# Kernel optimization log

Hardware: AMD Instinct MI355X
Metric: run time of the kernel (lower is better)

## Reference

```python
import jax, jax.numpy as jnp
import numpy as np

DIM = 1024
HEADS = 16
DIM_HEAD = 64
B, N = 2, 2048
EPS_NORM = 1e-12  # F.normalize clamp


def setup_inputs() -> dict:
    key = jax.random.key(0)
    k1, k2, k3 = jax.random.split(key, 3)
    x = jax.random.normal(k1, (B, N, DIM), dtype=jnp.float32)
    gamma = jnp.ones((DIM,), dtype=jnp.float32)
    w_qkv = jax.random.normal(k2, (DIM, 3 * HEADS * DIM_HEAD), dtype=jnp.float32) * (DIM ** -0.5)
    w_out = jax.random.normal(k3, (HEADS * DIM_HEAD, DIM), dtype=jnp.float32) * (DIM ** -0.5)
    return {"x": x, "gamma": gamma, "w_qkv": w_qkv, "w_out": w_out}


def reference(x, gamma, w_qkv, w_out):
    b, n, dim = x.shape
    h, dh = HEADS, DIM_HEAD
    # RMSNorm: F.normalize(x, dim=-1) * sqrt(dim) * gamma
    norm = jnp.maximum(jnp.linalg.norm(x, axis=-1, keepdims=True), EPS_NORM)
    normed = x / norm * (dim ** 0.5) * gamma
    # qkv projection (no bias)
    qkv = normed @ w_qkv  # [b, n, 3*h*dh]
    qkv = qkv.reshape(b, n, 3, h, dh)
    q = qkv[:, :, 0].transpose(0, 2, 1, 3)  # [b, h, n, dh]
    k = qkv[:, :, 1].transpose(0, 2, 1, 3)
    v = qkv[:, :, 2].transpose(0, 2, 1, 3)
    q = q * (dh ** -0.5)
    # attention scores
    sim = jnp.einsum('bhid,bhjd->bhij', q, k)
    mask_value = -jnp.finfo(sim.dtype).max
    # causal mask: triu with offset j - i + 1 (here i == j == n -> offset 1)
    causal_mask = jnp.triu(jnp.ones((n, n), dtype=bool), 1)
    sim = jnp.where(causal_mask, mask_value, sim)
    attn = jax.nn.softmax(sim, axis=-1)
    out = jnp.einsum('bhij,bhjd->bhid', attn, v)
    out = out.transpose(0, 2, 1, 3).reshape(b, n, h * dh)
    return out @ w_out
```

## Files before the change

kernel.cpp:

```cpp
#include <hip/hip_runtime.h>
#include <hip/hip_bf16.h>

typedef unsigned short u16;
using bf16x8 = __attribute__((ext_vector_type(8))) short;
using f32x4  = __attribute__((ext_vector_type(4))) float;
using f32x16 = __attribute__((ext_vector_type(16))) float;
using u32x4  = __attribute__((ext_vector_type(4))) unsigned int;

constexpr int B_ = 2, N_ = 2048, DIM_ = 1024, H_ = 16, DH_ = 64;
constexpr int M_ = B_ * N_;
constexpr int NCQ = 3 * H_ * DH_;

__device__ inline u16 f2bf(float f) {
  union { float f; unsigned u; } v{f};
  unsigned r = v.u + 0x7FFF + ((v.u >> 16) & 1);
  return (u16)(r >> 16);
}

__device__ __forceinline__ void st_pair(u16* p0, u16* p1, float a, float b) {
  unsigned w;
  asm("v_cvt_pk_bf16_f32 %0, %1, %2" : "=v"(w) : "v"(a), "v"(b));
  *p0 = (u16)w;
  *p1 = (u16)(w >> 16);
}

__device__ __forceinline__ void gload16(const u16* g, u16* l) {
  __builtin_amdgcn_global_load_lds(
      (const __attribute__((address_space(1))) unsigned int*)g,
      (__attribute__((address_space(3))) unsigned int*)l, 16, 0, 0);
}

__global__ void __launch_bounds__(256) rmsnorm_kernel(const float* __restrict__ x,
                                                      const float* __restrict__ gamma,
                                                      u16* __restrict__ out) {
  int row = blockIdx.x;
  int t = threadIdx.x;
  const float4 v = reinterpret_cast<const float4*>(x + (size_t)row * DIM_)[t];
  float ss = v.x * v.x + v.y * v.y + v.z * v.z + v.w * v.w;
#pragma unroll
  for (int o = 32; o; o >>= 1) ss += __shfl_down(ss, o, 64);
  __shared__ float partial[4];
  int wid = t >> 6, lane = t & 63;
  if (lane == 0) partial[wid] = ss;
  __syncthreads();
  float tot = partial[0] + partial[1] + partial[2] + partial[3];
  float norm = fmaxf(sqrtf(tot), 1e-12f);
  float scale = 32.0f / norm;
  const float4 g = reinterpret_cast<const float4*>(gamma)[t];
  ushort4 o4;
  o4.x = f2bf(v.x * scale * g.x);
  o4.y = f2bf(v.y * scale * g.y);
  o4.z = f2bf(v.z * scale * g.z);
  o4.w = f2bf(v.w * scale * g.w);
  reinterpret_cast<ushort4*>(out + (size_t)row * DIM_)[t] = o4;
}

__global__ void __launch_bounds__(256) transpose_w_kernel(const float* __restrict__ W,
                                                          u16* __restrict__ WT,
                                                          int K, int Nc) {
  __shared__ float tile[32][33];
  int bc = blockIdx.x * 32;
  int bk = blockIdx.y * 32;
  int tx = threadIdx.x & 31, ty = threadIdx.x >> 5;
#pragma unroll
  for (int r = ty; r < 32; r += 8)
    tile[r][tx] = W[(size_t)(bk + r) * Nc + bc + tx];
  __syncthreads();
#pragma unroll
  for (int r = ty; r < 32; r += 8)
    WT[(size_t)(bc + r) * K + bk + tx] = f2bf(tile[tx][r]);
}

template <int MODE>
__global__ void __launch_bounds__(256) gemm2_kernel(const u16* __restrict__ A,
                                                    const u16* __restrict__ BT,
                                                    void* __restrict__ Cv,
                                                    u16* __restrict__ q_s,
                                                    u16* __restrict__ k_s,
                                                    u16* __restrict__ vt,
                                                    int M, int Nc, int K) {
  __shared__ alignas(16) u16 smem[16384];
  int tid = threadIdx.x;
  int lane = tid & 63, wid = tid >> 6;
  int lr = lane & 15, g = lane >> 4;
  int am0 = (wid >> 1) * 64;
  int bn0 = (wid & 1) * 64;
  int rbase_a = blockIdx.y * 128;
  int rbase_b = blockIdx.x * 128;

  int lineo = tid >> 3;
  int p = tid & 7;
  f32x4 acc[4][4] = {};

#define GSTAGE(base_, src_, rb_, k0_) do {                                           \
    _Pragma("unroll")                                                                \
    for (int c = 0; c < 2; c++) {                                                    \
      int line = c * 32 + lineo;                                                     \
      int sp = p ^ (line & 7);                                                       \
      int row = 2 * line + (sp >> 2);                                                \
      int j = sp & 3;                                                                \
      gload16(src_ + (size_t)(rb_ + row) * K + (k0_) + j * 8,                        \
              (base_) + c * 2048 + wid * 512);                                       \
    }                                                                                \
  } while (0)

#define STAGE(ib_, k0_) do {                                                         \
    GSTAGE(smem + (ib_) * 4096, A, rbase_a, k0_);                                    \
    GSTAGE(smem + 8192 + (ib_) * 4096, BT, rbase_b, k0_);                            \
  } while (0)

  int steps = K >> 5;
  STAGE(0, 0);
  for (int t = 0; t < steps; ++t) {
    int ibuf = t & 1;
    if (t + 1 < steps) {
      STAGE(ibuf ^ 1, (t + 1) * 32);
      asm volatile("s_waitcnt vmcnt(4)" ::: "memory");
    } else {
      asm volatile("s_waitcnt vmcnt(0)" ::: "memory");
    }
    __builtin_amdgcn_s_barrier();
    __builtin_amdgcn_sched_barrier(0);

    const char* ab = (const char*)(smem + ibuf * 4096);
    const char* bb = (const char*)(smem + 8192 + ibuf * 4096);
    bf16x8 a[4], b[4];
#pragma unroll
    for (int mi = 0; mi < 4; mi++) {
      int row = am0 + mi * 16 + lr;
      int byte = (row >> 1) * 128 + ((((row & 1) << 2) + g) ^ ((row >> 1) & 7)) * 16;
      a[mi] = *reinterpret_cast<const bf16x8*>(ab + byte);
    }
#pragma unroll
    for (int ni = 0; ni < 4; ni++) {
      int row = bn0 + ni * 16 + lr;
      int byte = (row >> 1) * 128 + ((((row & 1) << 2) + g) ^ ((row >> 1) & 7)) * 16;
      b[ni] = *reinterpret_cast<const bf16x8*>(bb + byte);
    }
#pragma unroll
    for (int mi = 0; mi < 4; mi++)
#pragma unroll
      for (int ni = 0; ni < 4; ni++)
        acc[mi][ni] = __builtin_amdgcn_mfma_f32_16x16x32_bf16(a[mi], b[ni], acc[mi][ni], 0, 0, 0);

    __builtin_amdgcn_sched_barrier(0);
    __builtin_amdgcn_s_barrier();
  }

  int orow = g * 4;
  if (MODE == 1) {
#pragma unroll
    for (int mi = 0; mi < 4; mi++)
#pragma unroll
      for (int ni = 0; ni < 4; ni++)
#pragma unroll
        for (int r = 0; r < 4; r++) {
          int row = rbase_a + am0 + 16 * mi + orow + r;
          int col = rbase_b + bn0 + 16 * ni + lr;
          ((float*)Cv)[(size_t)row * Nc + col] = acc[mi][ni][r];
        }
  } else {
    int colbase = rbase_b + bn0;
    int region = colbase >> 10;
    int head = (colbase >> 6) & 15;
    const float QS = 0.125f * 1.4426950408889634f;
    if (region < 2) {
#pragma unroll
      for (int mi = 0; mi < 4; mi++)
#pragma unroll
        for (int ni = 0; ni < 4; ni++)
#pragma unroll
          for (int r = 0; r < 4; r += 2) {
            int row = rbase_a + am0 + 16 * mi + orow + r;
            int n = row & 2047, bb_ = row >> 11;
            float v0 = acc[mi][ni][r], v1 = acc[mi][ni][r + 1];
            size_t d0 = ((size_t)(bb_ * 16 + head) * 2048 + n) * 64 + 16 * ni + lr;
            if (region == 0)
              st_pair(q_s + d0, q_s + d0 + 64, v0 * QS, v1 * QS);
            else
              st_pair(k_s + d0, k_s + d0 + 64, v0, v1);
          }
    } else {
      u16* tlds = smem + wid * 4096;
      int n_base = (rbase_a + am0) & 2047;
      int bq = (rbase_a + am0) >> 11;
#pragma unroll
      for (int mi = 0; mi < 4; mi++)
#pragma unroll
        for (int ni = 0; ni < 4; ni++) {
          int n_loc = mi * 16 + orow;
          int dh_loc = ni * 16 + lr;
          unsigned w0, w1;
          asm("v_cvt_pk_bf16_f32 %0, %1, %2"
              : "=v"(w0) : "v"(acc[mi][ni][0]), "v"(acc[mi][ni][1]));
          asm("v_cvt_pk_bf16_f32 %0, %1, %2"
              : "=v"(w1) : "v"(acc[mi][ni][2]), "v"(acc[mi][ni][3]));
          int byte = dh_loc * 128 + ((n_loc * 2) ^ ((dh_loc & 7) << 4));
          uint2 val; val.x = w0; val.y = w1;
          *reinterpret_cast<uint2*>((char*)tlds + byte) = val;
        }
#pragma unroll
      for (int it = 0; it < 8; it++) {
        int dh_loc = it * 8 + (lane >> 3);
        int n8 = (lane & 7) * 8;
        int byte = dh_loc * 128 + ((n8 * 2) ^ ((dh_loc & 7) << 4));
        bf16x8 v = *reinterpret_cast<const bf16x8*>((const char*)tlds + byte);
        size_t dst = ((size_t)(bq * 16 + head) * 64 + dh_loc) * 2048 + n_base + n8;
        *reinterpret_cast<bf16x8*>(vt + dst) = v;
      }
    }
  }
#undef STAGE
#undef GSTAGE
}

__global__ void __launch_bounds__(128) attn7_kernel(const u16* __restrict__ q_s,
                                                    const u16* __restrict__ k_s,
                                                    const u16* __restrict__ vt,
                                                    u16* __restrict__ ao) {
  __shared__ alignas(16) u16 smem[16384];
  int tid = threadIdx.x;
  int lane = tid & 63, myhalf = tid >> 6;
  int q31 = lane & 31, hi = lane >> 5;
  int blk = blockIdx.x;
  int bh = blk & 31;
  int jq = 63 - (blk >> 5);
  int b = bh >> 4, h = bh & 15;
  const u16* qp = q_s + (size_t)bh * N_ * DH_;
  const u16* kp = k_s + (size_t)bh * N_ * DH_;
  const u16* vp = vt + (size_t)bh * DH_ * N_;
  int q0w = jq * 32;
  int qi = q0w + q31;
  int steps = (jq >> 1) + 1;

  bf16x8 qf[4];
#pragma unroll
  for (int c = 0; c < 4; c++)
    qf[c] = *reinterpret_cast<const bf16x8*>(qp + (size_t)(q0w + q31) * 64 + c * 16 + hi * 8);

  f32x16 o0 = {}, o1 = {};
  float lsum = 0.f;

  int srow = lane >> 3;
  int scol = (lane & 7) ^ srow;

#define STAGE(ib_, kv0_) do {                                                                \
    _Pragma("unroll")                                                                        \
    for (int cc = 0; cc < 4; cc++) {                                                         \
      int c = myhalf * 4 + cc;                                                               \
      gload16(kp + (size_t)((kv0_) + c * 8 + srow) * 64 + scol * 8,                          \
              smem + (ib_) * 4096 + c * 512);                                                \
      gload16(vp + (size_t)(c * 8 + srow) * N_ + (kv0_) + scol * 8,                          \
              smem + 8192 + (ib_) * 4096 + c * 512);                                         \
    }                                                                                        \
  } while (0)

  STAGE(0, 0);

  for (int t = 0; t < steps; ++t) {
    int ibuf = t & 1;
    if (t + 1 < steps) {
      STAGE(ibuf ^ 1, (t + 1) * 64);
      asm volatile("s_waitcnt vmcnt(8)" ::: "memory");
    } else {
      asm volatile("s_waitcnt vmcnt(0)" ::: "memory");
    }
    __builtin_amdgcn_s_barrier();
    __builtin_amdgcn_sched_barrier(0);

    const u16* kb = smem + ibuf * 4096;
    const u16* vb = smem + 8192 + ibuf * 4096;
    int kv = t * 64 + myhalf * 32;
    if (kv <= q0w + 31) {
      f32x16 st = {};
      int krow = myhalf * 32 + q31;
      int ksw = (krow & 7) << 4;
      __builtin_amdgcn_s_setprio(1);
#pragma unroll
      for (int c = 0; c < 4; c++) {
        bf16x8 kf = *reinterpret_cast<const bf16x8*>(
            (const char*)kb + krow * 128 + (((c * 2 + hi) * 16) ^ ksw));
        st = __builtin_amdgcn_mfma_f32_32x32x16_bf16(kf, qf[c], st, 0, 0, 0);
      }
      __builtin_amdgcn_s_setprio(0);
      float p[16];
      bool diag = (kv + 31 > q0w);
      if (diag) {
#pragma unroll
        for (int r = 0; r < 16; r++) {
          int key = kv + (r & 3) + 8 * (r >> 2) + 4 * hi;
          float e = __builtin_amdgcn_exp2f(st[r]);
          p[r] = (key > qi) ? 0.f : e;
        }
      } else {
#pragma unroll
        for (int r = 0; r < 16; r++) p[r] = __builtin_amdgcn_exp2f(st[r]);
      }
#pragma unroll
      for (int r = 0; r < 16; r++) lsum += p[r];
      unsigned cw0[4], cw1[4];
#pragma unroll
      for (int jj = 0; jj < 4; jj++) {
        asm("v_cvt_pk_bf16_f32 %0, %1, %2" : "=v"(cw0[jj]) : "v"(p[4 * jj]), "v"(p[4 * jj + 1]));
        asm("v_cvt_pk_bf16_f32 %0, %1, %2" : "=v"(cw1[jj]) : "v"(p[4 * jj + 2]), "v"(p[4 * jj + 3]));
      }
#pragma unroll
      for (int kc = 0; kc < 2; kc++) {
        unsigned c0a = cw0[2 * kc], c0b = cw0[2 * kc + 1];
        unsigned c1a = cw1[2 * kc], c1b = cw1[2 * kc + 1];
        unsigned sel0 = hi ? c0a : c0b;
        unsigned sel1 = hi ? c1a : c1b;
        unsigned r0 = (unsigned)__shfl_xor((int)sel0, 32, 64);
        unsigned r1 = (unsigned)__shfl_xor((int)sel1, 32, 64);
        u32x4 w;
        w[0] = hi ? r0 : c0a;
        w[1] = hi ? r1 : c1a;
        w[2] = hi ? c0b : r0;
        w[3] = hi ? c1b : r1;
        bf16x8 pa = __builtin_bit_cast(bf16x8, w);
        int slot = (myhalf * 4 + kc * 2 + hi) * 16;
        int vsw = (q31 & 7) << 4;
        bf16x8 vf0 = *reinterpret_cast<const bf16x8*>(
            (const char*)vb + q31 * 128 + (slot ^ vsw));
        bf16x8 vf1 = *reinterpret_cast<const bf16x8*>(
            (const char*)vb + (32 + q31) * 128 + (slot ^ vsw));
        __builtin_amdgcn_s_setprio(1);
        o0 = __builtin_amdgcn_mfma_f32_32x32x16_bf16(pa, vf0, o0, 0, 0, 0);
        o1 = __builtin_amdgcn_mfma_f32_32x32x16_bf16(pa, vf1, o1, 0, 0, 0);
        __builtin_amdgcn_s_setprio(0);
      }
    }
    __builtin_amdgcn_sched_barrier(0);
    __builtin_amdgcn_s_barrier();
  }

  __syncthreads();
  float lc = lsum + __shfl_xor(lsum, 32, 64);
  float* cb = (float*)smem;
  if (myhalf) {
#pragma unroll
    for (int r = 0; r < 16; r++) {
      cb[r * 64 + lane] = o0[r];
      cb[(16 + r) * 64 + lane] = o1[r];
    }
    cb[2048 + lane] = lc;
  }
  __syncthreads();
  if (!myhalf) {
#pragma unroll
    for (int r = 0; r < 16; r++) {
      o0[r] += cb[r * 64 + lane];
      o1[r] += cb[(16 + r) * 64 + lane];
    }
    float ltot = fmaxf(lc + cb[2048 + lane], 1e-30f);
    float linv = 1.0f / ltot;
#pragma unroll
    for (int r = 0; r < 16; r += 2) {
      int qrow0 = (r & 3) + 8 * (r >> 2) + 4 * hi;
      float li0 = __shfl(linv, qrow0, 64);
      float li1 = __shfl(linv, qrow0 + 1, 64);
      size_t base0 = (size_t)(b * N_ + q0w + qrow0) * 1024 + h * 64;
      st_pair(ao + base0 + q31, ao + base0 + 1024 + q31, o0[r] * li0, o0[r + 1] * li1);
      st_pair(ao + base0 + 32 + q31, ao + base0 + 1024 + 32 + q31, o1[r] * li0, o1[r + 1] * li1);
    }
  }
#undef STAGE
}

extern "C" void kernel_launch(void* const* d_in, const int* in_sizes, int n_in,
                              void* d_out, int out_size, void* d_ws, size_t ws_size,
                              hipStream_t stream) {
  const float* x = (const float*)d_in[0];
  const float* gamma = (const float*)d_in[1];
  const float* w_qkv = (const float*)d_in[2];
  const float* w_out = (const float*)d_in[3];
  float* out = (float*)d_out;

  char* p = (char*)d_ws;
  u16* normed = (u16*)p; p += (size_t)M_ * DIM_ * 2;
  u16* wt_qkv = (u16*)p; p += (size_t)NCQ * DIM_ * 2;
  u16* wt_out = (u16*)p; p += (size_t)DIM_ * DIM_ * 2;
  u16* k_s = (u16*)p;    p += (size_t)M_ * DIM_ * 2;
  u16* vt = (u16*)p;     p += (size_t)M_ * DIM_ * 2;
  u16* q_s = (u16*)p;    p += (size_t)M_ * DIM_ * 2;
  u16* ao = (u16*)p;     p += (size_t)M_ * DIM_ * 2;

  hipLaunchKernelGGL(rmsnorm_kernel, dim3(M_), dim3(256), 0, stream, x, gamma, normed);
  hipLaunchKernelGGL(transpose_w_kernel, dim3(NCQ / 32, DIM_ / 32), dim3(256), 0, stream,
                     w_qkv, wt_qkv, DIM_, NCQ);
  hipLaunchKernelGGL(transpose_w_kernel, dim3(DIM_ / 32, DIM_ / 32), dim3(256), 0, stream,
                     w_out, wt_out, DIM_, DIM_);
  hipLaunchKernelGGL(gemm2_kernel<2>, dim3(NCQ / 128, M_ / 128), dim3(256), 0, stream,
                     normed, wt_qkv, nullptr, q_s, k_s, vt, M_, NCQ, DIM_);
  hipLaunchKernelGGL(attn7_kernel, dim3(B_ * H_ * (N_ / 32)), dim3(128), 0, stream,
                     q_s, k_s, vt, ao);
  hipLaunchKernelGGL(gemm2_kernel<1>, dim3(DIM_ / 128, M_ / 128), dim3(256), 0, stream,
                     ao, wt_out, (void*)out, nullptr, nullptr, nullptr, M_, DIM_, DIM_);
}
```

Baseline: 116.5 us.

## Split attention KV tiles per wave and remap GEMM blocks across XCDs

```diff
diff --git a/kernel.cpp b/kernel.cpp
--- a/kernel.cpp
+++ b/kernel.cpp
@@ -85,8 +85,12 @@
   int lr = lane & 15, g = lane >> 4;
   int am0 = (wid >> 1) * 64;
   int bn0 = (wid & 1) * 64;
-  int rbase_a = blockIdx.y * 128;
-  int rbase_b = blockIdx.x * 128;
+  int nwg = gridDim.x;
+  int lwg = (blockIdx.x & 7) * (nwg >> 3) + (blockIdx.x >> 3);
+  int by = lwg & 31;
+  int bx = lwg >> 5;
+  int rbase_a = by * 128;
+  int rbase_b = bx * 128;
 
   int lineo = tid >> 3;
   int p = tid & 7;
@@ -214,13 +218,13 @@
 #undef GSTAGE
 }
 
-__global__ void __launch_bounds__(128) attn7_kernel(const u16* __restrict__ q_s,
-                                                    const u16* __restrict__ k_s,
-                                                    const u16* __restrict__ vt,
-                                                    u16* __restrict__ ao) {
-  __shared__ alignas(16) u16 smem[16384];
+__global__ void __launch_bounds__(128) attn10_kernel(const u16* __restrict__ q_s,
+                                                     const u16* __restrict__ k_s,
+                                                     const u16* __restrict__ vt,
+                                                     u16* __restrict__ ao) {
+  __shared__ alignas(16) u16 smem[8192];
   int tid = threadIdx.x;
-  int lane = tid & 63, myhalf = tid >> 6;
+  int lane = tid & 63, par = tid >> 6;
   int q31 = lane & 31, hi = lane >> 5;
   int blk = blockIdx.x;
   int bh = blk & 31;
@@ -231,7 +235,7 @@
   const u16* vp = vt + (size_t)bh * DH_ * N_;
   int q0w = jq * 32;
   int qi = q0w + q31;
-  int steps = (jq >> 1) + 1;
+  int nt = (jq >= par) ? (((jq - par) >> 1) + 1) : 0;
 
   bf16x8 qf[4];
 #pragma unroll
@@ -241,50 +245,50 @@
   f32x16 o0 = {}, o1 = {};
   float lsum = 0.f;
 
+  u16* sw = smem + par * 4096;
   int srow = lane >> 3;
   int scol = (lane & 7) ^ srow;
-
-#define STAGE(ib_, kv0_) do {                                                                \
-    _Pragma("unroll")                                                                        \
-    for (int cc = 0; cc < 4; cc++) {                                                         \
-      int c = myhalf * 4 + cc;                                                               \
-      gload16(kp + (size_t)((kv0_) + c * 8 + srow) * 64 + scol * 8,                          \
-              smem + (ib_) * 4096 + c * 512);                                                \
-      gload16(vp + (size_t)(c * 8 + srow) * N_ + (kv0_) + scol * 8,                          \
-              smem + 8192 + (ib_) * 4096 + c * 512);                                         \
-    }                                                                                        \
+  const u16* vbase0 = vp + (size_t)q31 * 2048 + hi * 8;
+  const u16* vbase1 = vbase0 + (size_t)32 * 2048;
+
+#define STAGEW(ib_, m_) do {                                                         \
+    _Pragma("unroll")                                                                \
+    for (int cc = 0; cc < 4; cc++)                                                   \
+      gload16(kp + (size_t)((m_) * 32 + cc * 8 + srow) * 64 + scol * 8,              \
+              sw + (ib_) * 2048 + cc * 512);                                         \
   } while (0)
 
-  STAGE(0, 0);
-
-  for (int t = 0; t < steps; ++t) {
-    int ibuf = t & 1;
-    if (t + 1 < steps) {
-      STAGE(ibuf ^ 1, (t + 1) * 64);
-      asm volatile("s_waitcnt vmcnt(8)" ::: "memory");
-    } else {
-      asm volatile("s_waitcnt vmcnt(0)" ::: "memory");
-    }
-    __builtin_amdgcn_s_barrier();
-    __builtin_amdgcn_sched_barrier(0);
-
-    const u16* kb = smem + ibuf * 4096;
-    const u16* vb = smem + 8192 + ibuf * 4096;
-    int kv = t * 64 + myhalf * 32;
-    if (kv <= q0w + 31) {
+  if (nt > 0) {
+    STAGEW(0, par);
+    for (int t = 0; t < nt; ++t) {
+      int m = 2 * t + par;
+      int kv = m * 32;
+      int ib = t & 1;
+      bf16x8 vf00 = *reinterpret_cast<const bf16x8*>(vbase0 + kv);
+      bf16x8 vf01 = *reinterpret_cast<const bf16x8*>(vbase0 + kv + 16);
+      bf16x8 vf10 = *reinterpret_cast<const bf16x8*>(vbase1 + kv);
+      bf16x8 vf11 = *reinterpret_cast<const bf16x8*>(vbase1 + kv + 16);
+      if (t + 1 < nt) {
+        STAGEW(ib ^ 1, m + 2);
+        asm volatile("s_waitcnt vmcnt(8)" ::: "memory");
+      } else {
+        asm volatile("s_waitcnt vmcnt(4)" ::: "memory");
+      }
+      __builtin_amdgcn_sched_barrier(0);
+
+      const char* kb = (const char*)(sw + ib * 2048);
       f32x16 st = {};
-      int krow = myhalf * 32 + q31;
-      int ksw = (krow & 7) << 4;
+      int ksw = (q31 & 7) << 4;
       __builtin_amdgcn_s_setprio(1);
 #pragma unroll
       for (int c = 0; c < 4; c++) {
         bf16x8 kf = *reinterpret_cast<const bf16x8*>(
-            (const char*)kb + krow * 128 + (((c * 2 + hi) * 16) ^ ksw));
+            kb + q31 * 128 + (((c * 2 + hi) * 16) ^ ksw));
         st = __builtin_amdgcn_mfma_f32_32x32x16_bf16(kf, qf[c], st, 0, 0, 0);
       }
       __builtin_amdgcn_s_setprio(0);
       float p[16];
-      bool diag = (kv + 31 > q0w);
+      bool diag = (t == nt - 1) && ((jq & 1) == par);
       if (diag) {
 #pragma unroll
         for (int r = 0; r < 16; r++) {
@@ -318,26 +322,18 @@
         w[2] = hi ? c0b : r0;
         w[3] = hi ? c1b : r1;
         bf16x8 pa = __builtin_bit_cast(bf16x8, w);
-        int slot = (myhalf * 4 + kc * 2 + hi) * 16;
-        int vsw = (q31 & 7) << 4;
-        bf16x8 vf0 = *reinterpret_cast<const bf16x8*>(
-            (const char*)vb + q31 * 128 + (slot ^ vsw));
-        bf16x8 vf1 = *reinterpret_cast<const bf16x8*>(
-            (const char*)vb + (32 + q31) * 128 + (slot ^ vsw));
         __builtin_amdgcn_s_setprio(1);
-        o0 = __builtin_amdgcn_mfma_f32_32x32x16_bf16(pa, vf0, o0, 0, 0, 0);
-        o1 = __builtin_amdgcn_mfma_f32_32x32x16_bf16(pa, vf1, o1, 0, 0, 0);
+        o0 = __builtin_amdgcn_mfma_f32_32x32x16_bf16(pa, kc ? vf01 : vf00, o0, 0, 0, 0);
+        o1 = __builtin_amdgcn_mfma_f32_32x32x16_bf16(pa, kc ? vf11 : vf10, o1, 0, 0, 0);
         __builtin_amdgcn_s_setprio(0);
       }
     }
-    __builtin_amdgcn_sched_barrier(0);
-    __builtin_amdgcn_s_barrier();
   }
 
   __syncthreads();
   float lc = lsum + __shfl_xor(lsum, 32, 64);
   float* cb = (float*)smem;
-  if (myhalf) {
+  if (par) {
 #pragma unroll
     for (int r = 0; r < 16; r++) {
       cb[r * 64 + lane] = o0[r];
@@ -346,7 +342,7 @@
     cb[2048 + lane] = lc;
   }
   __syncthreads();
-  if (!myhalf) {
+  if (!par) {
 #pragma unroll
     for (int r = 0; r < 16; r++) {
       o0[r] += cb[r * 64 + lane];
@@ -364,7 +360,7 @@
       st_pair(ao + base0 + 32 + q31, ao + base0 + 1024 + 32 + q31, o1[r] * li0, o1[r + 1] * li1);
     }
   }
-#undef STAGE
+#undef STAGEW
 }
 
 extern "C" void kernel_launch(void* const* d_in, const int* in_sizes, int n_in,
@@ -390,10 +386,10 @@
                      w_qkv, wt_qkv, DIM_, NCQ);
   hipLaunchKernelGGL(transpose_w_kernel, dim3(DIM_ / 32, DIM_ / 32), dim3(256), 0, stream,
                      w_out, wt_out, DIM_, DIM_);
-  hipLaunchKernelGGL(gemm2_kernel<2>, dim3(NCQ / 128, M_ / 128), dim3(256), 0, stream,
+  hipLaunchKernelGGL(gemm2_kernel<2>, dim3((NCQ / 128) * (M_ / 128)), dim3(256), 0, stream,
                      normed, wt_qkv, nullptr, q_s, k_s, vt, M_, NCQ, DIM_);
-  hipLaunchKernelGGL(attn7_kernel, dim3(B_ * H_ * (N_ / 32)), dim3(128), 0, stream,
+  hipLaunchKernelGGL(attn10_kernel, dim3(B_ * H_ * (N_ / 32)), dim3(128), 0, stream,
                      q_s, k_s, vt, ao);
-  hipLaunchKernelGGL(gemm2_kernel<1>, dim3(DIM_ / 128, M_ / 128), dim3(256), 0, stream,
+  hipLaunchKernelGGL(gemm2_kernel<1>, dim3((DIM_ / 128) * (M_ / 128)), dim3(256), 0, stream,
                      ao, wt_out, (void*)out, nullptr, nullptr, nullptr, M_, DIM_, DIM_);
 }
```

Measured after the change: 117.9 us. About the same (+1.2%).
